# Optimization experiments

Hardware: AMD Instinct MI355X
Metric: run time of the kernel (lower is better)

Reference implementation:

```python
import jax, jax.numpy as jnp
import numpy as np

N = 10000      # num nodes
E = 320000     # num edges
IN = 256       # in_dim
MP = 256       # mp_width
FL = 512       # fl_width
OUT = 64       # out_dim


def setup_inputs() -> dict:
    key = jax.random.key(0)
    ks = jax.random.split(key, 20)
    inp = {}
    inp["x"] = jax.random.normal(ks[0], (N, IN), dtype=jnp.float32)
    inp["edge_index"] = jax.random.randint(ks[1], (2, E), 0, N, dtype=jnp.int64)
    # iMP (frozen) linear layers: weight ~ N(0, 1) per nn.init.normal_(std=1.0)
    inp["mp_w0"] = jax.random.normal(ks[2], (IN, MP), dtype=jnp.float32)
    inp["mp_b0"] = jax.random.uniform(ks[3], (MP,), minval=-1.0, maxval=1.0) / np.sqrt(IN)
    inp["mp_w1"] = jax.random.normal(ks[4], (MP, MP), dtype=jnp.float32)
    inp["mp_b1"] = jax.random.uniform(ks[5], (MP,), minval=-1.0, maxval=1.0) / np.sqrt(MP)
    inp["mp_w2"] = jax.random.normal(ks[6], (MP, MP), dtype=jnp.float32)
    inp["mp_b2"] = jax.random.uniform(ks[7], (MP,), minval=-1.0, maxval=1.0) / np.sqrt(MP)
    # FC layers (torch default Linear init scale ~ 1/sqrt(fan_in))
    inp["fc_w0"] = jax.random.normal(ks[8], (MP, FL), dtype=jnp.float32) / np.sqrt(MP)
    inp["fc_b0"] = jnp.zeros((FL,), dtype=jnp.float32)
    inp["fc_w1"] = jax.random.normal(ks[9], (FL, FL), dtype=jnp.float32) / np.sqrt(FL)
    inp["fc_b1"] = jnp.zeros((FL,), dtype=jnp.float32)
    # injection projections
    inp["inj_w0"] = jax.random.normal(ks[10], (MP, FL), dtype=jnp.float32) / np.sqrt(MP)
    inp["inj_b0"] = jnp.zeros((FL,), dtype=jnp.float32)
    inp["inj_w1"] = jax.random.normal(ks[11], (MP, FL), dtype=jnp.float32) / np.sqrt(MP)
    inp["inj_b1"] = jnp.zeros((FL,), dtype=jnp.float32)
    inp["alpha"] = jnp.array(1.0, dtype=jnp.float32)
    inp["out_w"] = jax.random.normal(ks[12], (FL, OUT), dtype=jnp.float32) / np.sqrt(FL)
    inp["out_b"] = jnp.zeros((OUT,), dtype=jnp.float32)
    return inp


def _imp(x, w, b, row, col, deg_inv):
    # h = relu(W x); h /= deg; Ah = scatter_add over row of h[col]
    h = jax.nn.relu(x @ w + b) * deg_inv[:, None]      # [N, out]
    return jnp.zeros_like(h).at[row].add(h[col])       # gather + scatter-add


def reference(x, edge_index, mp_w0, mp_b0, mp_w1, mp_b1, mp_w2, mp_b2,
              fc_w0, fc_b0, fc_w1, fc_b1, inj_w0, inj_b0, inj_w1, inj_b1,
              alpha, out_w, out_b):
    row, col = edge_index[0], edge_index[1]
    deg = jax.ops.segment_sum(jnp.ones((E,), x.dtype), col, num_segments=N)
    # nodes with deg==0 never appear in col so clamping does not change output
    deg_inv = 1.0 / jnp.maximum(deg, 1.0)

    h = _imp(x, mp_w0, mp_b0, row, col, deg_inv)
    h = _imp(h, mp_w1, mp_b1, row, col, deg_inv)
    h = _imp(h, mp_w2, mp_b2, row, col, deg_inv)

    x_inject = h
    h = alpha * (jax.nn.relu(h) @ fc_w0 + fc_b0) + (x_inject @ inj_w0 + inj_b0)
    h = alpha * (jax.nn.relu(h) @ fc_w1 + fc_b1) + (x_inject @ inj_w1 + inj_b1)
    return h @ out_w + out_b
```

## Files before the change

kernel.cpp:

```cpp
#include <hip/hip_runtime.h>

#define N_NODES 10000
#define N_EDGES 320000
#define MPAD 10112
#define NBIN 10048
#define CHUNK 2048
#define NCH 157

typedef unsigned short u16;
typedef short bf16x8 __attribute__((ext_vector_type(8)));
typedef float f32x4 __attribute__((ext_vector_type(4)));

__device__ __forceinline__ u16 f2b(float f) {
  unsigned u = __builtin_bit_cast(unsigned, f);
  unsigned r = u + 0x7fffu + ((u >> 16) & 1u);
  return (u16)(r >> 16);
}
__device__ __forceinline__ unsigned pack2(float a, float b) {
  return (unsigned)f2b(a) | ((unsigned)f2b(b) << 16);
}
__device__ __forceinline__ float blo(unsigned u) { return __builtin_bit_cast(float, u << 16); }
__device__ __forceinline__ float bhi(unsigned u) { return __builtin_bit_cast(float, u & 0xffff0000u); }

__global__ void prep(
    const float* __restrict__ x,
    const float* __restrict__ w0, const float* __restrict__ w1, const float* __restrict__ w2,
    const float* __restrict__ fcw0, const float* __restrict__ injw0,
    const float* __restrict__ fcw1, const float* __restrict__ injw1,
    const float* __restrict__ outw,
    const float* __restrict__ fcb0, const float* __restrict__ injb0,
    const float* __restrict__ fcb1, const float* __restrict__ injb1,
    const float* __restrict__ alpha_p,
    u16* __restrict__ xb, u16* __restrict__ w0t, u16* __restrict__ w1t, u16* __restrict__ w2t,
    u16* __restrict__ wc1t, u16* __restrict__ wc2t, u16* __restrict__ owt,
    float* __restrict__ bias1, float* __restrict__ bias2)
{
  long i = (long)blockIdx.x * 256 + threadIdx.x;
  const float alpha = alpha_p[0];
  if (i < 640000L) {
    float4 v = ((const float4*)x)[i];
    uint2 o;
    o.x = pack2(v.x, v.y);
    o.y = pack2(v.z, v.w);
    *(uint2*)(xb + 4 * i) = o;
    return;
  }
  i -= 640000L;
  if (i < 65536) { w0t[i] = f2b(w0[(i & 255) * 256 + (i >> 8)]); return; }
  i -= 65536;
  if (i < 65536) { w1t[i] = f2b(w1[(i & 255) * 256 + (i >> 8)]); return; }
  i -= 65536;
  if (i < 65536) { w2t[i] = f2b(w2[(i & 255) * 256 + (i >> 8)]); return; }
  i -= 65536;
  if (i < 262144) {
    int n = (int)(i >> 9), k = (int)(i & 511);
    float v = (k < 256) ? alpha * fcw0[k * 512 + n] : injw0[(k - 256) * 512 + n];
    wc1t[i] = f2b(v); return;
  }
  i -= 262144;
  if (i < 393216) {
    int n = (int)(i / 768), k = (int)(i % 768);
    float v = (k < 512) ? alpha * fcw1[k * 512 + n] : injw1[(k - 512) * 512 + n];
    wc2t[i] = f2b(v); return;
  }
  i -= 393216;
  if (i < 32768) {
    int n = (int)(i >> 9), k = (int)(i & 511);
    owt[i] = f2b(outw[k * 64 + n]); return;
  }
  i -= 32768;
  if (i < 512) { bias1[i] = alpha * fcb0[i] + injb0[i]; return; }
  i -= 512;
  if (i < 512) { bias2[i] = alpha * fcb1[i] + injb1[i]; return; }
}

__global__ __launch_bounds__(256) void edge_hist(const int* __restrict__ ei,
                                                 int* __restrict__ histR,
                                                 int* __restrict__ histC) {
  __shared__ int hr[NBIN], hc[NBIN];
  const int ch = blockIdx.x, t = threadIdx.x;
  for (int i = t; i < NBIN; i += 256) { hr[i] = 0; hc[i] = 0; }
  __syncthreads();
  const int e0 = ch * CHUNK;
#pragma unroll
  for (int j = 0; j < CHUNK; j += 256) {
    int e = e0 + j + t;
    if (e < N_EDGES) {
      atomicAdd(&hr[ei[e]], 1);
      atomicAdd(&hc[ei[N_EDGES + e]], 1);
    }
  }
  __syncthreads();
  for (int i = t; i < NBIN; i += 256) {
    histR[(size_t)ch * NBIN + i] = hr[i];
    histC[(size_t)ch * NBIN + i] = hc[i];
  }
}

__global__ __launch_bounds__(256) void col_scan(const int* __restrict__ histR,
                                                const int* __restrict__ histC,
                                                int* __restrict__ chunkoff,
                                                int* __restrict__ cntR,
                                                float* __restrict__ deg_inv) {
  int r = blockIdx.x * 256 + threadIdx.x;
  if (r >= MPAD) return;
  if (r >= NBIN) { deg_inv[r] = 1.0f; return; }
  int run = 0, dg = 0;
#pragma unroll 4
  for (int ch = 0; ch < NCH; ++ch) {
    chunkoff[(size_t)ch * NBIN + r] = run;
    run += histR[(size_t)ch * NBIN + r];
    dg  += histC[(size_t)ch * NBIN + r];
  }
  cntR[r] = run;
  deg_inv[r] = 1.0f / (float)(dg > 1 ? dg : 1);
}

__global__ __launch_bounds__(1024) void row_scan(const int* __restrict__ cntR,
                                                 int* __restrict__ row_ptr) {
  const int t = threadIdx.x;
  const int i0 = t * 10;
  int v[10];
  int s = 0;
#pragma unroll
  for (int i = 0; i < 10; ++i) {
    int id = i0 + i;
    v[i] = (id < NBIN) ? cntR[id] : 0;
    s += v[i];
  }
  int lane = t & 63, wid = t >> 6;
  int incl = s;
#pragma unroll
  for (int off = 1; off < 64; off <<= 1) {
    int y = __shfl_up(incl, off, 64);
    if (lane >= off) incl += y;
  }
  __shared__ int wsum[16], wexc[16];
  if (lane == 63) wsum[wid] = incl;
  __syncthreads();
  if (t == 0) {
    int run = 0;
#pragma unroll
    for (int i = 0; i < 16; ++i) { wexc[i] = run; run += wsum[i]; }
  }
  __syncthreads();
  int run = wexc[wid] + incl - s;
#pragma unroll
  for (int i = 0; i < 10; ++i) {
    int id = i0 + i;
    if (id <= N_NODES) row_ptr[id] = run;
    run += v[i];
  }
}

__global__ __launch_bounds__(256) void place_edges(const int* __restrict__ ei,
                                                   const int* __restrict__ chunkoff,
                                                   const int* __restrict__ row_ptr,
                                                   int* __restrict__ csr) {
  __shared__ int cur[NBIN];
  const int ch = blockIdx.x, t = threadIdx.x;
  const int* co = chunkoff + (size_t)ch * NBIN;
  for (int i = t; i < NBIN; i += 256) cur[i] = co[i];
  __syncthreads();
  const int e0 = ch * CHUNK;
#pragma unroll
  for (int j = 0; j < CHUNK; j += 256) {
    int e = e0 + j + t;
    if (e < N_EDGES) {
      int r = ei[e];
      int c = ei[N_EDGES + e];
      int rank = atomicAdd(&cur[r], 1);
      csr[row_ptr[r] + rank] = c;
    }
  }
}

template<int K, bool RELU, bool SCALE, bool F32OUT>
__global__ __launch_bounds__(128) void gemm64(
    const u16* __restrict__ A, int lda,
    const u16* __restrict__ Bt,
    const float* __restrict__ bias,
    const float* __restrict__ scale,
    u16* __restrict__ Cb, float* __restrict__ Cf, int ldc)
{
  __shared__ u16 As[64 * 72];
  __shared__ u16 Bs[64 * 72];
  const int tid = threadIdx.x;
  const int m0 = blockIdx.x * 64;
  const int n0 = blockIdx.y * 64;
  const int wave = tid >> 6;
  const int lane = tid & 63;
  const int wr = wave * 32;
  const int lm = lane & 15;
  const int koff = (lane >> 4) * 8;

  const int srow = tid >> 2;
  const int scol = (tid & 3) * 16;
  const u16* Ag0 = A + (size_t)(m0 + srow) * lda + scol;
  const u16* Ag1 = A + (size_t)(m0 + srow + 32) * lda + scol;
  const u16* Bg0 = Bt + (size_t)(n0 + srow) * K + scol;
  const u16* Bg1 = Bt + (size_t)(n0 + srow + 32) * K + scol;
  u16* Asw0 = &As[srow * 72 + scol];
  u16* Asw1 = &As[(srow + 32) * 72 + scol];
  u16* Bsw0 = &Bs[srow * 72 + scol];
  u16* Bsw1 = &Bs[(srow + 32) * 72 + scol];

  f32x4 acc[2][4] = {};

  int4 pa0 = *(const int4*)(Ag0),     pa1 = *(const int4*)(Ag0 + 8);
  int4 pa2 = *(const int4*)(Ag1),     pa3 = *(const int4*)(Ag1 + 8);
  int4 pb0 = *(const int4*)(Bg0),     pb1 = *(const int4*)(Bg0 + 8);
  int4 pb2 = *(const int4*)(Bg1),     pb3 = *(const int4*)(Bg1 + 8);

#pragma unroll
  for (int kb = 0; kb < K; kb += 64) {
    __syncthreads();
    *(int4*)Asw0 = pa0; *(int4*)(Asw0 + 8) = pa1;
    *(int4*)Asw1 = pa2; *(int4*)(Asw1 + 8) = pa3;
    *(int4*)Bsw0 = pb0; *(int4*)(Bsw0 + 8) = pb1;
    *(int4*)Bsw1 = pb2; *(int4*)(Bsw1 + 8) = pb3;
    __syncthreads();
    if (kb + 64 < K) {
      pa0 = *(const int4*)(Ag0 + kb + 64); pa1 = *(const int4*)(Ag0 + kb + 72);
      pa2 = *(const int4*)(Ag1 + kb + 64); pa3 = *(const int4*)(Ag1 + kb + 72);
      pb0 = *(const int4*)(Bg0 + kb + 64); pb1 = *(const int4*)(Bg0 + kb + 72);
      pb2 = *(const int4*)(Bg1 + kb + 64); pb3 = *(const int4*)(Bg1 + kb + 72);
    }
#pragma unroll
    for (int ks = 0; ks < 2; ++ks) {
      bf16x8 af[2], bf[4];
#pragma unroll
      for (int mi = 0; mi < 2; ++mi)
        af[mi] = *(const bf16x8*)&As[(wr + mi * 16 + lm) * 72 + ks * 32 + koff];
#pragma unroll
      for (int ni = 0; ni < 4; ++ni)
        bf[ni] = *(const bf16x8*)&Bs[(ni * 16 + lm) * 72 + ks * 32 + koff];
#pragma unroll
      for (int mi = 0; mi < 2; ++mi)
#pragma unroll
        for (int ni = 0; ni < 4; ++ni)
          acc[mi][ni] = __builtin_amdgcn_mfma_f32_16x16x32_bf16(af[mi], bf[ni], acc[mi][ni], 0, 0, 0);
    }
  }

  const int q4 = (lane >> 4) * 4;
#pragma unroll
  for (int mi = 0; mi < 2; ++mi) {
#pragma unroll
    for (int ni = 0; ni < 4; ++ni) {
      const int gc = n0 + ni * 16 + lm;
      const float bv = bias[gc];
#pragma unroll
      for (int r = 0; r < 4; ++r) {
        const int gr = m0 + wr + mi * 16 + q4 + r;
        float v = acc[mi][ni][r] + bv;
        if (RELU) v = fmaxf(v, 0.f);
        if (SCALE) v *= scale[gr];
        if (F32OUT) {
          if (gr < N_NODES) Cf[(size_t)gr * ldc + gc] = v;
        } else {
          Cb[(size_t)gr * ldc + gc] = f2b(v);
        }
      }
    }
  }
}

__global__ __launch_bounds__(256) void aggregate(
    const u16* __restrict__ tmp, const int* __restrict__ row_ptr,
    const int* __restrict__ csr, u16* __restrict__ out0,
    u16* __restrict__ A1, u16* __restrict__ A2, int mode)
{
  const int wv = threadIdx.x >> 6;
  const int lane = threadIdx.x & 63;
  const int r = blockIdx.x * 4 + wv;
  const int half = lane >> 5;
  const int q = lane & 31;
  const int beg = row_ptr[r], end = row_ptr[r + 1];
  const size_t feat = (size_t)q * 16;
  const char* tb = (const char*)tmp;

  float s0 = 0.f, s1 = 0.f, s2 = 0.f, s3 = 0.f, s4 = 0.f, s5 = 0.f, s6 = 0.f, s7 = 0.f;
  int i = beg;
  for (; i + 8 <= end; i += 8) {
    uint4 v[4];
#pragma unroll
    for (int j = 0; j < 4; ++j)
      v[j] = *(const uint4*)(tb + (size_t)csr[i + 2 * j + half] * 512 + feat);
#pragma unroll
    for (int j = 0; j < 4; ++j) {
      s0 += blo(v[j].x); s1 += bhi(v[j].x); s2 += blo(v[j].y); s3 += bhi(v[j].y);
      s4 += blo(v[j].z); s5 += bhi(v[j].z); s6 += blo(v[j].w); s7 += bhi(v[j].w);
    }
  }
  for (; i < end; i += 2) {
    int id = i + half;
    if (id < end) {
      uint4 v = *(const uint4*)(tb + (size_t)csr[id] * 512 + feat);
      s0 += blo(v.x); s1 += bhi(v.x); s2 += blo(v.y); s3 += bhi(v.y);
      s4 += blo(v.z); s5 += bhi(v.z); s6 += blo(v.w); s7 += bhi(v.w);
    }
  }
  const int src = lane ^ 32;
  s0 += __shfl(s0, src, 64); s1 += __shfl(s1, src, 64);
  s2 += __shfl(s2, src, 64); s3 += __shfl(s3, src, 64);
  s4 += __shfl(s4, src, 64); s5 += __shfl(s5, src, 64);
  s6 += __shfl(s6, src, 64); s7 += __shfl(s7, src, 64);

  if (half == 0) {
    uint4 pv;
    pv.x = pack2(s0, s1); pv.y = pack2(s2, s3);
    pv.z = pack2(s4, s5); pv.w = pack2(s6, s7);
    if (mode == 0) {
      *(uint4*)((char*)out0 + (size_t)r * 512 + feat) = pv;
    } else {
      uint4 pr;
      pr.x = pack2(fmaxf(s0, 0.f), fmaxf(s1, 0.f));
      pr.y = pack2(fmaxf(s2, 0.f), fmaxf(s3, 0.f));
      pr.z = pack2(fmaxf(s4, 0.f), fmaxf(s5, 0.f));
      pr.w = pack2(fmaxf(s6, 0.f), fmaxf(s7, 0.f));
      *(uint4*)((char*)A1 + (size_t)r * 1024 + feat) = pr;
      *(uint4*)((char*)A1 + (size_t)r * 1024 + 512 + feat) = pv;
      *(uint4*)((char*)A2 + (size_t)r * 1536 + 1024 + feat) = pv;
    }
  }
}

extern "C" void kernel_launch(void* const* d_in, const int* in_sizes, int n_in,
                              void* d_out, int out_size, void* d_ws, size_t ws_size,
                              hipStream_t stream) {
  const float* x      = (const float*)d_in[0];
  const int*   ei     = (const int*)d_in[1];
  const float* mp_w0  = (const float*)d_in[2];
  const float* mp_b0  = (const float*)d_in[3];
  const float* mp_w1  = (const float*)d_in[4];
  const float* mp_b1  = (const float*)d_in[5];
  const float* mp_w2  = (const float*)d_in[6];
  const float* mp_b2  = (const float*)d_in[7];
  const float* fc_w0  = (const float*)d_in[8];
  const float* fc_b0  = (const float*)d_in[9];
  const float* fc_w1  = (const float*)d_in[10];
  const float* fc_b1  = (const float*)d_in[11];
  const float* inj_w0 = (const float*)d_in[12];
  const float* inj_b0 = (const float*)d_in[13];
  const float* inj_w1 = (const float*)d_in[14];
  const float* inj_b1 = (const float*)d_in[15];
  const float* alpha  = (const float*)d_in[16];
  const float* out_w  = (const float*)d_in[17];
  const float* out_b  = (const float*)d_in[18];
  float* out = (float*)d_out;

  char* p = (char*)d_ws;
  auto carve = [&](size_t bytes) -> void* {
    void* r = (void*)p;
    p += (bytes + 255) & ~(size_t)255;
    return r;
  };
  int*   histR    = (int*)carve((size_t)NCH * NBIN * 4);
  int*   histC    = (int*)carve((size_t)NCH * NBIN * 4);
  int*   chunkoff = (int*)carve((size_t)NCH * NBIN * 4);
  int*   cntR     = (int*)carve(NBIN * 4);
  int*   row_ptr  = (int*)carve((N_NODES + 1) * 4);
  int*   csr      = (int*)carve((size_t)N_EDGES * 4);
  float* deg_inv  = (float*)carve(MPAD * 4);
  float* bias1    = (float*)carve(512 * 4);
  float* bias2    = (float*)carve(512 * 4);
  u16* xb   = (u16*)carve((size_t)MPAD * 256 * 2);
  u16* w0t  = (u16*)carve(65536 * 2);
  u16* w1t  = (u16*)carve(65536 * 2);
  u16* w2t  = (u16*)carve(65536 * 2);
  u16* wc1t = (u16*)carve(262144 * 2);
  u16* wc2t = (u16*)carve(393216 * 2);
  u16* owt  = (u16*)carve(32768 * 2);
  u16* tmp  = (u16*)carve((size_t)MPAD * 256 * 2);
  u16* h    = (u16*)carve((size_t)MPAD * 256 * 2);
  u16* A1   = (u16*)carve((size_t)MPAD * 512 * 2);
  u16* A2   = (u16*)carve((size_t)MPAD * 768 * 2);
  u16* C2   = (u16*)carve((size_t)MPAD * 512 * 2);

  prep<<<5960, 256, 0, stream>>>(x, mp_w0, mp_w1, mp_w2, fc_w0, inj_w0, fc_w1, inj_w1,
                                 out_w, fc_b0, inj_b0, fc_b1, inj_b1, alpha,
                                 xb, w0t, w1t, w2t, wc1t, wc2t, owt, bias1, bias2);
  edge_hist<<<NCH, 256, 0, stream>>>(ei, histR, histC);
  col_scan<<<(MPAD + 255) / 256, 256, 0, stream>>>(histR, histC, chunkoff, cntR, deg_inv);
  row_scan<<<1, 1024, 0, stream>>>(cntR, row_ptr);
  place_edges<<<NCH, 256, 0, stream>>>(ei, chunkoff, row_ptr, csr);

  dim3 gmp(MPAD / 64, 4), gfc(MPAD / 64, 8), go(MPAD / 64, 1);
  gemm64<256, true, true, false><<<gmp, 128, 0, stream>>>(xb, 256, w0t, mp_b0, deg_inv, tmp, nullptr, 256);
  aggregate<<<2500, 256, 0, stream>>>(tmp, row_ptr, csr, h, nullptr, nullptr, 0);
  gemm64<256, true, true, false><<<gmp, 128, 0, stream>>>(h, 256, w1t, mp_b1, deg_inv, tmp, nullptr, 256);
  aggregate<<<2500, 256, 0, stream>>>(tmp, row_ptr, csr, h, nullptr, nullptr, 0);
  gemm64<256, true, true, false><<<gmp, 128, 0, stream>>>(h, 256, w2t, mp_b2, deg_inv, tmp, nullptr, 256);
  aggregate<<<2500, 256, 0, stream>>>(tmp, row_ptr, csr, nullptr, A1, A2, 1);
  gemm64<512, true, false, false><<<gfc, 128, 0, stream>>>(A1, 512, wc1t, bias1, nullptr, A2, nullptr, 768);
  gemm64<768, false, false, false><<<gfc, 128, 0, stream>>>(A2, 768, wc2t, bias2, nullptr, C2, nullptr, 512);
  gemm64<512, false, false, true><<<go, 128, 0, stream>>>(C2, 512, owt, out_b, nullptr, nullptr, out, 64);
}
```

Before: 267.9 us.

## Fold fc_w1/inj_w1 into output projection and merge prep with edge histogram

Precomputes the product of the second FC and injection weights with the output weight, giving a 768x64 fused weight and fused bias. This removes the 768->512 GEMM and the intermediate C2 buffer, leaving one small 768->64 GEMM. It also merges the weight/input conversion kernel and the edge histogram into one launch, split by block index, to save a launch and overlap the two. The weight product is computed with a scalar fp32 loop in the prep kernel, and doing the fusion in bf16 changes rounding slightly.

```diff
diff --git a/kernel.cpp b/kernel.cpp
--- a/kernel.cpp
+++ b/kernel.cpp
@@ -6,6 +6,8 @@
 #define NBIN 10048
 #define CHUNK 2048
 #define NCH 157
+#define PREP_BLOCKS 259
+#define PREP_TOT 1148480L
 
 typedef unsigned short u16;
 typedef short bf16x8 __attribute__((ext_vector_type(8)));
@@ -22,78 +24,90 @@
 __device__ __forceinline__ float blo(unsigned u) { return __builtin_bit_cast(float, u << 16); }
 __device__ __forceinline__ float bhi(unsigned u) { return __builtin_bit_cast(float, u & 0xffff0000u); }
 
-__global__ void prep(
-    const float* __restrict__ x,
-    const float* __restrict__ w0, const float* __restrict__ w1, const float* __restrict__ w2,
-    const float* __restrict__ fcw0, const float* __restrict__ injw0,
-    const float* __restrict__ fcw1, const float* __restrict__ injw1,
-    const float* __restrict__ outw,
-    const float* __restrict__ fcb0, const float* __restrict__ injb0,
-    const float* __restrict__ fcb1, const float* __restrict__ injb1,
-    const float* __restrict__ alpha_p,
-    u16* __restrict__ xb, u16* __restrict__ w0t, u16* __restrict__ w1t, u16* __restrict__ w2t,
-    u16* __restrict__ wc1t, u16* __restrict__ wc2t, u16* __restrict__ owt,
-    float* __restrict__ bias1, float* __restrict__ bias2)
-{
-  long i = (long)blockIdx.x * 256 + threadIdx.x;
-  const float alpha = alpha_p[0];
-  if (i < 640000L) {
-    float4 v = ((const float4*)x)[i];
-    uint2 o;
-    o.x = pack2(v.x, v.y);
-    o.y = pack2(v.z, v.w);
-    *(uint2*)(xb + 4 * i) = o;
+struct PP {
+  const float *x; const int *ei;
+  const float *w0, *w1, *w2, *fcw0, *injw0, *fcw1, *injw1, *outw;
+  const float *fcb0, *injb0, *fcb1, *injb1, *alpha, *outb;
+  u16 *xb, *w0t, *w1t, *w2t, *wc1t, *wft;
+  float *bias1, *bf;
+  int *histR, *histC;
+};
+
+__global__ __launch_bounds__(256) void prep_hist(PP P) {
+  __shared__ int sh[2 * NBIN];
+  const int tid = threadIdx.x, bid = blockIdx.x;
+  const float alpha = P.alpha[0];
+
+  if (bid < NCH) {
+    for (int i = tid; i < 2 * NBIN; i += 256) sh[i] = 0;
+    __syncthreads();
+    const int e0 = bid * CHUNK;
+    for (int j = tid; j < CHUNK; j += 256) {
+      int e = e0 + j;
+      if (e < N_EDGES) {
+        atomicAdd(&sh[P.ei[e]], 1);
+        atomicAdd(&sh[NBIN + P.ei[N_EDGES + e]], 1);
+      }
+    }
+    __syncthreads();
+    for (int i = tid; i < NBIN; i += 256) {
+      P.histR[(size_t)bid * NBIN + i] = sh[i];
+      P.histC[(size_t)bid * NBIN + i] = sh[NBIN + i];
+    }
     return;
   }
-  i -= 640000L;
-  if (i < 65536) { w0t[i] = f2b(w0[(i & 255) * 256 + (i >> 8)]); return; }
-  i -= 65536;
-  if (i < 65536) { w1t[i] = f2b(w1[(i & 255) * 256 + (i >> 8)]); return; }
-  i -= 65536;
-  if (i < 65536) { w2t[i] = f2b(w2[(i & 255) * 256 + (i >> 8)]); return; }
-  i -= 65536;
-  if (i < 262144) {
-    int n = (int)(i >> 9), k = (int)(i & 511);
-    float v = (k < 256) ? alpha * fcw0[k * 512 + n] : injw0[(k - 256) * 512 + n];
-    wc1t[i] = f2b(v); return;
-  }
-  i -= 262144;
-  if (i < 393216) {
-    int n = (int)(i / 768), k = (int)(i % 768);
-    float v = (k < 512) ? alpha * fcw1[k * 512 + n] : injw1[(k - 512) * 512 + n];
-    wc2t[i] = f2b(v); return;
-  }
-  i -= 393216;
-  if (i < 32768) {
-    int n = (int)(i >> 9), k = (int)(i & 511);
-    owt[i] = f2b(outw[k * 64 + n]); return;
-  }
-  i -= 32768;
-  if (i < 512) { bias1[i] = alpha * fcb0[i] + injb0[i]; return; }
-  i -= 512;
-  if (i < 512) { bias2[i] = alpha * fcb1[i] + injb1[i]; return; }
-}
-
-__global__ __launch_bounds__(256) void edge_hist(const int* __restrict__ ei,
-                                                 int* __restrict__ histR,
-                                                 int* __restrict__ histC) {
-  __shared__ int hr[NBIN], hc[NBIN];
-  const int ch = blockIdx.x, t = threadIdx.x;
-  for (int i = t; i < NBIN; i += 256) { hr[i] = 0; hc[i] = 0; }
-  __syncthreads();
-  const int e0 = ch * CHUNK;
-#pragma unroll
-  for (int j = 0; j < CHUNK; j += 256) {
-    int e = e0 + j + t;
-    if (e < N_EDGES) {
-      atomicAdd(&hr[ei[e]], 1);
-      atomicAdd(&hc[ei[N_EDGES + e]], 1);
-    }
-  }
-  __syncthreads();
-  for (int i = t; i < NBIN; i += 256) {
-    histR[(size_t)ch * NBIN + i] = hr[i];
-    histC[(size_t)ch * NBIN + i] = hc[i];
+
+  const long stride = (long)PREP_BLOCKS * 256;
+  for (long ii = (long)(bid - NCH) * 256 + tid; ii < PREP_TOT; ii += stride) {
+    long i = ii;
+    if (i < 640000L) {
+      float4 v = ((const float4*)P.x)[i];
+      uint2 o;
+      o.x = pack2(v.x, v.y);
+      o.y = pack2(v.z, v.w);
+      *(uint2*)(P.xb + 4 * i) = o;
+      continue;
+    }
+    i -= 640000L;
+    if (i < 65536) { P.w0t[i] = f2b(P.w0[(i & 255) * 256 + (i >> 8)]); continue; }
+    i -= 65536;
+    if (i < 65536) { P.w1t[i] = f2b(P.w1[(i & 255) * 256 + (i >> 8)]); continue; }
+    i -= 65536;
+    if (i < 65536) { P.w2t[i] = f2b(P.w2[(i & 255) * 256 + (i >> 8)]); continue; }
+    i -= 65536;
+    if (i < 262144) {
+      int n = (int)(i >> 9), k = (int)(i & 511);
+      float v = (k < 256) ? alpha * P.fcw0[k * 512 + n] : P.injw0[(k - 256) * 512 + n];
+      P.wc1t[i] = f2b(v); continue;
+    }
+    i -= 262144;
+    if (i < 49152) {
+      int n = (int)(i & 63), k = (int)(i >> 6);
+      float acc = 0.f;
+      if (k < 512) {
+        const float* fr = P.fcw1 + (size_t)k * 512;
+#pragma unroll 8
+        for (int j = 0; j < 512; ++j) acc += fr[j] * P.outw[j * 64 + n];
+        acc *= alpha;
+      } else {
+        const float* ir = P.injw1 + (size_t)(k - 512) * 512;
+#pragma unroll 8
+        for (int j = 0; j < 512; ++j) acc += ir[j] * P.outw[j * 64 + n];
+      }
+      P.wft[n * 768 + k] = f2b(acc);
+      continue;
+    }
+    i -= 49152;
+    if (i < 64) {
+      float acc = P.outb[i];
+#pragma unroll 8
+      for (int j = 0; j < 512; ++j)
+        acc += (alpha * P.fcb1[j] + P.injb1[j]) * P.outw[j * 64 + i];
+      P.bf[i] = acc;
+      continue;
+    }
+    i -= 64;
+    if (i < 512) { P.bias1[i] = alpha * P.fcb0[i] + P.injb0[i]; continue; }
   }
 }
 
@@ -329,26 +343,7 @@
 extern "C" void kernel_launch(void* const* d_in, const int* in_sizes, int n_in,
                               void* d_out, int out_size, void* d_ws, size_t ws_size,
                               hipStream_t stream) {
-  const float* x      = (const float*)d_in[0];
-  const int*   ei     = (const int*)d_in[1];
-  const float* mp_w0  = (const float*)d_in[2];
-  const float* mp_b0  = (const float*)d_in[3];
-  const float* mp_w1  = (const float*)d_in[4];
-  const float* mp_b1  = (const float*)d_in[5];
-  const float* mp_w2  = (const float*)d_in[6];
-  const float* mp_b2  = (const float*)d_in[7];
-  const float* fc_w0  = (const float*)d_in[8];
-  const float* fc_b0  = (const float*)d_in[9];
-  const float* fc_w1  = (const float*)d_in[10];
-  const float* fc_b1  = (const float*)d_in[11];
-  const float* inj_w0 = (const float*)d_in[12];
-  const float* inj_b0 = (const float*)d_in[13];
-  const float* inj_w1 = (const float*)d_in[14];
-  const float* inj_b1 = (const float*)d_in[15];
-  const float* alpha  = (const float*)d_in[16];
-  const float* out_w  = (const float*)d_in[17];
-  const float* out_b  = (const float*)d_in[18];
-  float* out = (float*)d_out;
+  const int* ei = (const int*)d_in[1];
 
   char* p = (char*)d_ws;
   auto carve = [&](size_t bytes) -> void* {
@@ -364,24 +359,46 @@
   int*   csr      = (int*)carve((size_t)N_EDGES * 4);
   float* deg_inv  = (float*)carve(MPAD * 4);
   float* bias1    = (float*)carve(512 * 4);
-  float* bias2    = (float*)carve(512 * 4);
+  float* bf       = (float*)carve(64 * 4);
   u16* xb   = (u16*)carve((size_t)MPAD * 256 * 2);
   u16* w0t  = (u16*)carve(65536 * 2);
   u16* w1t  = (u16*)carve(65536 * 2);
   u16* w2t  = (u16*)carve(65536 * 2);
   u16* wc1t = (u16*)carve(262144 * 2);
-  u16* wc2t = (u16*)carve(393216 * 2);
-  u16* owt  = (u16*)carve(32768 * 2);
+  u16* wft  = (u16*)carve(49152 * 2);
   u16* tmp  = (u16*)carve((size_t)MPAD * 256 * 2);
   u16* h    = (u16*)carve((size_t)MPAD * 256 * 2);
-  u16* A1   = (u16*)carve((size_t)MPAD * 512 * 2);
-  u16* A2   = (u16*)carve((size_t)MPAD * 768 * 2);
-  u16* C2   = (u16*)carve((size_t)MPAD * 512 * 2);
-
-  prep<<<5960, 256, 0, stream>>>(x, mp_w0, mp_w1, mp_w2, fc_w0, inj_w0, fc_w1, inj_w1,
-                                 out_w, fc_b0, inj_b0, fc_b1, inj_b1, alpha,
-                                 xb, w0t, w1t, w2t, wc1t, wc2t, owt, bias1, bias2);
-  edge_hist<<<NCH, 256, 0, stream>>>(ei, histR, histC);
+  u16* cat1 = (u16*)carve((size_t)MPAD * 512 * 2);
+  u16* cat2 = (u16*)carve((size_t)MPAD * 768 * 2);
+
+  PP pp;
+  pp.x = (const float*)d_in[0];
+  pp.ei = ei;
+  pp.w0 = (const float*)d_in[2];
+  pp.w1 = (const float*)d_in[4];
+  pp.w2 = (const float*)d_in[6];
+  pp.fcw0 = (const float*)d_in[8];
+  pp.fcw1 = (const float*)d_in[10];
+  pp.injw0 = (const float*)d_in[12];
+  pp.injw1 = (const float*)d_in[14];
+  pp.outw = (const float*)d_in[17];
+  pp.fcb0 = (const float*)d_in[9];
+  pp.injb0 = (const float*)d_in[13];
+  pp.fcb1 = (const float*)d_in[11];
+  pp.injb1 = (const float*)d_in[15];
+  pp.alpha = (const float*)d_in[16];
+  pp.outb = (const float*)d_in[18];
+  pp.xb = xb; pp.w0t = w0t; pp.w1t = w1t; pp.w2t = w2t;
+  pp.wc1t = wc1t; pp.wft = wft;
+  pp.bias1 = bias1; pp.bf = bf;
+  pp.histR = histR; pp.histC = histC;
+
+  const float* mp_b0 = (const float*)d_in[3];
+  const float* mp_b1 = (const float*)d_in[5];
+  const float* mp_b2 = (const float*)d_in[7];
+  float* out = (float*)d_out;
+
+  prep_hist<<<NCH + PREP_BLOCKS, 256, 0, stream>>>(pp);
   col_scan<<<(MPAD + 255) / 256, 256, 0, stream>>>(histR, histC, chunkoff, cntR, deg_inv);
   row_scan<<<1, 1024, 0, stream>>>(cntR, row_ptr);
   place_edges<<<NCH, 256, 0, stream>>>(ei, chunkoff, row_ptr, csr);
@@ -392,8 +409,7 @@
   gemm64<256, true, true, false><<<gmp, 128, 0, stream>>>(h, 256, w1t, mp_b1, deg_inv, tmp, nullptr, 256);
   aggregate<<<2500, 256, 0, stream>>>(tmp, row_ptr, csr, h, nullptr, nullptr, 0);
   gemm64<256, true, true, false><<<gmp, 128, 0, stream>>>(h, 256, w2t, mp_b2, deg_inv, tmp, nullptr, 256);
-  aggregate<<<2500, 256, 0, stream>>>(tmp, row_ptr, csr, nullptr, A1, A2, 1);
-  gemm64<512, true, false, false><<<gfc, 128, 0, stream>>>(A1, 512, wc1t, bias1, nullptr, A2, nullptr, 768);
-  gemm64<768, false, false, false><<<gfc, 128, 0, stream>>>(A2, 768, wc2t, bias2, nullptr, C2, nullptr, 512);
-  gemm64<512, false, false, true><<<go, 128, 0, stream>>>(C2, 512, owt, out_b, nullptr, nullptr, out, 64);
-}
+  aggregate<<<2500, 256, 0, stream>>>(tmp, row_ptr, csr, nullptr, cat1, cat2, 1);
+  gemm64<512, true, false, false><<<gfc, 128, 0, stream>>>(cat1, 512, wc1t, bias1, nullptr, cat2, nullptr, 768);
+  gemm64<768, false, false, true><<<go, 128, 0, stream>>>(cat2, 768, wft, bf, nullptr, nullptr, out, 64);
+}
```

Result: no change. 265.4 us (-0.9%).
